# Kernel optimization log

Measured on AMD Instinct MI355X. Metric: run time of the kernel, lower is better.

The kernel has to match this reference:

```python
import jax, jax.numpy as jnp
import numpy as np

B, S, F = 4, 2048, 8
D, H, L, FF = 256, 8, 2, 1024
DH = D // H
NSK, NPAT = 2000, 64
DQ = D // 4  # pattern/feat sub-embedding width


def setup_inputs() -> dict:
    key = jax.random.key(0)
    ks = jax.random.split(key, 32)
    r = lambda i, shape: jax.random.normal(ks[i], shape, jnp.float32) * 0.02
    return {
        'interactions': jax.random.randint(ks[0], (B, S), 0, 2 * NSK),
        'patterns': jax.random.randint(ks[1], (B, S), 0, NPAT),
        'forget_features': jax.random.normal(ks[2], (B, S, F), jnp.float32),
        'inter_emb': r(3, (2 * NSK, D)),
        'pattern_emb': r(4, (NPAT, DQ)),
        'feat_W': r(5, (F, DQ)), 'feat_b': jnp.zeros((DQ,), jnp.float32),
        'in_W': r(6, (D + 2 * DQ, D)), 'in_b': jnp.zeros((D,), jnp.float32),
        'time_W': r(7, (1, D)), 'time_b': jnp.zeros((D,), jnp.float32),
        'pos_W': r(8, (1, D)), 'pos_b': jnp.zeros((D,), jnp.float32),
        'Wq': r(9, (L, D, H, DH)), 'bq': jnp.zeros((L, H, DH), jnp.float32),
        'Wk': r(10, (L, D, H, DH)), 'bk': jnp.zeros((L, H, DH), jnp.float32),
        'Wv': r(11, (L, D, H, DH)), 'bv': jnp.zeros((L, H, DH), jnp.float32),
        'Wo': r(12, (L, H, DH, D)), 'bo': jnp.zeros((L, D), jnp.float32),
        'kerple_p': jnp.full((L, H, 1, 1), 0.5, jnp.float32),
        'kerple_a': jnp.zeros((L, H, 1, 1), jnp.float32),
        'ln1_g': jnp.ones((L, D), jnp.float32), 'ln1_b': jnp.zeros((L, D), jnp.float32),
        'ln2_g': jnp.ones((L, D), jnp.float32), 'ln2_b': jnp.zeros((L, D), jnp.float32),
        'ffn_W1': r(13, (L, D, FF)), 'ffn_b1': jnp.zeros((L, FF), jnp.float32),
        'ffn_W2': r(14, (L, FF, D)), 'ffn_b2': jnp.zeros((L, D), jnp.float32),
        'out_W': r(15, (D, NSK)), 'out_b': jnp.zeros((NSK,), jnp.float32),
    }


def _ln(x, g, b, eps=1e-6):
    m = jnp.mean(x, -1, keepdims=True)
    v = jnp.mean(jnp.square(x - m), -1, keepdims=True)
    return g * (x - m) * jax.lax.rsqrt(v + eps) + b


def reference(interactions, patterns, forget_features, inter_emb, pattern_emb,
              feat_W, feat_b, in_W, in_b, time_W, time_b, pos_W, pos_b,
              Wq, bq, Wk, bk, Wv, bv, Wo, bo, kerple_p, kerple_a,
              ln1_g, ln1_b, ln2_g, ln2_b, ffn_W1, ffn_b1, ffn_W2, ffn_b2,
              out_W, out_b):
    inter_e = inter_emb[interactions]                      # [B,S,D]
    pat_e = pattern_emb[patterns]                          # [B,S,D/4]
    feat_e = forget_features @ feat_W + feat_b             # [B,S,D/4]
    x = jnp.concatenate([inter_e, pat_e, feat_e], -1) @ in_W + in_b  # [B,S,D]
    elapsed = forget_features[:, :, 0:1]
    time_enc = jnp.tanh(elapsed @ time_W + time_b)
    pos = jnp.arange(S, dtype=jnp.float32)[None, :, None] / jnp.float32(S)
    pos_enc = pos @ pos_W + pos_b
    x = x + time_enc + pos_enc

    positions = jnp.arange(S, dtype=jnp.float32)
    dist = jnp.maximum(positions[:, None] - positions[None, :], 0.0)  # [S,S]
    causal_bias = jnp.triu(jnp.full((S, S), -1e9, jnp.float32), 1)    # [S,S]
    inv_sqrt_dh = 1.0 / jnp.sqrt(jnp.float32(DH))

    for i in range(L):
        p = jax.nn.softplus(kerple_p[i])                   # [H,1,1]
        a = jax.nn.softplus(kerple_a[i])
        bias = causal_bias[None] - p * jnp.log1p(a * dist[None])  # [H,S,S]
        q = jnp.einsum('bsd,dhk->bshk', x, Wq[i]) + bq[i]
        k = jnp.einsum('bsd,dhk->bshk', x, Wk[i]) + bk[i]
        v = jnp.einsum('bsd,dhk->bshk', x, Wv[i]) + bv[i]
        scores = jnp.einsum('bshk,bthk->bhst', q, k) * inv_sqrt_dh + bias[None]
        attn = jax.nn.softmax(scores, axis=-1)
        o = jnp.einsum('bhst,bthk->bshk', attn, v)
        attn_out = jnp.einsum('bshk,hkd->bsd', o, Wo[i]) + bo[i]
        x = _ln(x + attn_out, ln1_g[i], ln1_b[i])
        h = jax.nn.gelu(x @ ffn_W1[i] + ffn_b1[i], approximate=False)
        ffn_out = h @ ffn_W2[i] + ffn_b2[i]
        x = _ln(x + ffn_out, ln2_g[i], ln2_b[i])
    return x @ out_W + out_b
```

## Files before the change

kernel.cpp:

```cpp
#include <hip/hip_runtime.h>
#include <math.h>

#define SEQ   2048
#define BATCH 4
#define NTOK  8192
#define DM    256
#define NHD   8
#define DHD   32
#define DFF   1024
#define NSKC  2000

typedef __attribute__((ext_vector_type(8))) short short8;
typedef __attribute__((ext_vector_type(4))) float f32x4;
typedef unsigned short ushort_t;

__device__ __forceinline__ ushort_t f2bf(float x) {
    union { float f; unsigned u; } c; c.f = x;
    unsigned r = c.u + 0x7FFFu + ((c.u >> 16) & 1u);
    return (ushort_t)(r >> 16);
}

struct ConvSeg { const float* src; ushort_t* dst; int K; int N; int Npad; };
struct ConvArgs { ConvSeg s[14]; };

__global__ __launch_bounds__(256) void convert_kernel(ConvArgs args) {
    ConvSeg sg = args.s[blockIdx.y];
    int e = blockIdx.x * 256 + threadIdx.x;
    int tot = sg.Npad * sg.K;
    if (e >= tot) return;
    int n = e / sg.K;
    int k = e - n * sg.K;
    float v = (n < sg.N) ? sg.src[(size_t)k * sg.N + n] : 0.0f;
    sg.dst[e] = f2bf(v);
}

__global__ __launch_bounds__(384) void concat_kernel(
    const int* __restrict__ interactions, const int* __restrict__ patterns,
    const float* __restrict__ ff, const float* __restrict__ inter_emb,
    const float* __restrict__ pattern_emb, const float* __restrict__ feat_W,
    const float* __restrict__ feat_b, ushort_t* __restrict__ out)
{
    int tok = blockIdx.x;
    int j = threadIdx.x;
    float v;
    if (j < 256) {
        v = inter_emb[(size_t)interactions[tok] * 256 + j];
    } else if (j < 320) {
        v = pattern_emb[patterns[tok] * 64 + (j - 256)];
    } else {
        int c = j - 320;
        float acc = feat_b[c];
#pragma unroll
        for (int f = 0; f < 8; f++) acc += ff[tok * 8 + f] * feat_W[f * 64 + c];
        v = acc;
    }
    out[(size_t)tok * 384 + j] = f2bf(v);
}

__global__ __launch_bounds__(256) void addenc_kernel(
    float* __restrict__ x, ushort_t* __restrict__ xb, const float* __restrict__ ff,
    const float* __restrict__ time_W, const float* __restrict__ time_b,
    const float* __restrict__ pos_W, const float* __restrict__ pos_b)
{
    int tok = blockIdx.x;
    int d = threadIdx.x;
    int s = tok & (SEQ - 1);
    float el = ff[tok * 8];
    float te = tanhf(el * time_W[d] + time_b[d]);
    float pe = ((float)s * (1.0f / (float)SEQ)) * pos_W[d] + pos_b[d];
    size_t idx = (size_t)tok * DM + d;
    float nv = x[idx] + te + pe;
    x[idx] = nv;
    xb[idx] = f2bf(nv);
}

__global__ __launch_bounds__(256) void ln_kernel(
    float* __restrict__ x, const float* __restrict__ r,
    const float* __restrict__ g, const float* __restrict__ b,
    ushort_t* __restrict__ xb)
{
    int tok = blockIdx.x;
    int d = threadIdx.x;
    size_t idx = (size_t)tok * DM + d;
    float v = x[idx] + r[idx];
    float s1 = v, s2 = v * v;
#pragma unroll
    for (int off = 32; off > 0; off >>= 1) {
        s1 += __shfl_down(s1, off, 64);
        s2 += __shfl_down(s2, off, 64);
    }
    __shared__ float red1[4], red2[4];
    int wid = d >> 6, lane = d & 63;
    if (lane == 0) { red1[wid] = s1; red2[wid] = s2; }
    __syncthreads();
    s1 = red1[0] + red1[1] + red1[2] + red1[3];
    s2 = red2[0] + red2[1] + red2[2] + red2[3];
    float mean = s1 * (1.0f / 256.0f);
    float var = s2 * (1.0f / 256.0f) - mean * mean;
    float inv = rsqrtf(var + 1e-6f);
    float nv = g[d] * (v - mean) * inv + b[d];
    x[idx] = nv;
    xb[idx] = f2bf(nv);
}

__global__ __launch_bounds__(256) void gemm_bf16(
    const ushort_t* __restrict__ A, const ushort_t* __restrict__ Bt,
    int M, int N, int K, int mode,
    float* __restrict__ Cf, ushort_t* __restrict__ Cb,
    ushort_t* __restrict__ Ck, ushort_t* __restrict__ Cv,
    const float* __restrict__ b0, const float* __restrict__ b1,
    const float* __restrict__ b2)
{
    __shared__ ushort_t As[128][40];
    __shared__ ushort_t Bs[64][40];
    int m0 = blockIdx.y * 128, n0 = blockIdx.x * 64;
    int tid = threadIdx.x;
    int wv = tid >> 6, lane = tid & 63;
    int quad = lane >> 4, l16 = lane & 15;
    int srow = tid >> 2, sc = (tid & 3) << 3;

    f32x4 acc[2][4];
#pragma unroll
    for (int i = 0; i < 2; i++)
#pragma unroll
        for (int j = 0; j < 4; j++) acc[i][j] = (f32x4){0.f, 0.f, 0.f, 0.f};

    uint4 pa0 = *(const uint4*)&A[(size_t)(m0 + srow) * K + sc];
    uint4 pa1 = *(const uint4*)&A[(size_t)(m0 + 64 + srow) * K + sc];
    uint4 pbb = *(const uint4*)&Bt[(size_t)(n0 + srow) * K + sc];

    int msub = wv * 32;
    for (int k0 = 0; k0 < K; k0 += 32) {
        __syncthreads();
        *(uint4*)&As[srow][sc] = pa0;
        *(uint4*)&As[64 + srow][sc] = pa1;
        *(uint4*)&Bs[srow][sc] = pbb;
        __syncthreads();
        if (k0 + 32 < K) {
            pa0 = *(const uint4*)&A[(size_t)(m0 + srow) * K + k0 + 32 + sc];
            pa1 = *(const uint4*)&A[(size_t)(m0 + 64 + srow) * K + k0 + 32 + sc];
            pbb = *(const uint4*)&Bt[(size_t)(n0 + srow) * K + k0 + 32 + sc];
        }
        short8 af0 = *(const short8*)&As[msub + l16][quad * 8];
        short8 af1 = *(const short8*)&As[msub + 16 + l16][quad * 8];
        short8 bf0 = *(const short8*)&Bs[l16][quad * 8];
        short8 bf1 = *(const short8*)&Bs[16 + l16][quad * 8];
        short8 bf2 = *(const short8*)&Bs[32 + l16][quad * 8];
        short8 bf3 = *(const short8*)&Bs[48 + l16][quad * 8];
        acc[0][0] = __builtin_amdgcn_mfma_f32_16x16x32_bf16(af0, bf0, acc[0][0], 0, 0, 0);
        acc[0][1] = __builtin_amdgcn_mfma_f32_16x16x32_bf16(af0, bf1, acc[0][1], 0, 0, 0);
        acc[0][2] = __builtin_amdgcn_mfma_f32_16x16x32_bf16(af0, bf2, acc[0][2], 0, 0, 0);
        acc[0][3] = __builtin_amdgcn_mfma_f32_16x16x32_bf16(af0, bf3, acc[0][3], 0, 0, 0);
        acc[1][0] = __builtin_amdgcn_mfma_f32_16x16x32_bf16(af1, bf0, acc[1][0], 0, 0, 0);
        acc[1][1] = __builtin_amdgcn_mfma_f32_16x16x32_bf16(af1, bf1, acc[1][1], 0, 0, 0);
        acc[1][2] = __builtin_amdgcn_mfma_f32_16x16x32_bf16(af1, bf2, acc[1][2], 0, 0, 0);
        acc[1][3] = __builtin_amdgcn_mfma_f32_16x16x32_bf16(af1, bf3, acc[1][3], 0, 0, 0);
    }

#pragma unroll
    for (int mt = 0; mt < 2; mt++) {
#pragma unroll
        for (int nt = 0; nt < 4; nt++) {
            int n = n0 + nt * 16 + l16;
#pragma unroll
            for (int r = 0; r < 4; r++) {
                int m = m0 + msub + mt * 16 + quad * 4 + r;
                float v = acc[mt][nt][r];
                if (mode == 0) {
                    Cf[(size_t)m * N + n] = v + b0[n];
                } else {
                    int which = n >> 8, idx = n & 255;
                    int hh = idx >> 5, d = idx & 31;
                    int s = m & (SEQ - 1), b = m >> 11;
                    if (which == 0)
                        Cb[(((size_t)(b * NHD + hh)) * SEQ + s) * DHD + d] = f2bf(v + b0[idx]);
                    else if (which == 1)
                        Ck[(((size_t)(b * NHD + hh)) * SEQ + s) * DHD + d] = f2bf(v + b1[idx]);
                    else
                        Cv[(((size_t)(b * NHD + hh)) * DHD + d) * SEQ + s] = f2bf(v + b2[idx]);
                }
            }
        }
    }
}

__global__ __launch_bounds__(256) void gemm_bf16_128(
    const ushort_t* __restrict__ A, const ushort_t* __restrict__ Bt,
    int M, int N, int K, int mode,
    float* __restrict__ Cf, ushort_t* __restrict__ Cb,
    const float* __restrict__ b0, int Nreal)
{
    __shared__ ushort_t As[128][40];
    __shared__ ushort_t Bs[128][40];
    int m0 = blockIdx.y * 128, n0 = blockIdx.x * 128;
    int tid = threadIdx.x;
    int wv = tid >> 6, lane = tid & 63;
    int quad = lane >> 4, l16 = lane & 15;
    int wm = (wv >> 1) * 64, wn = (wv & 1) * 64;
    int srow = tid >> 1, sc = (tid & 1) << 4;

    f32x4 acc[4][4];
#pragma unroll
    for (int i = 0; i < 4; i++)
#pragma unroll
        for (int j = 0; j < 4; j++) acc[i][j] = (f32x4){0.f, 0.f, 0.f, 0.f};

    uint4 pa0 = *(const uint4*)&A[(size_t)(m0 + srow) * K + sc];
    uint4 pa1 = *(const uint4*)&A[(size_t)(m0 + srow) * K + sc + 8];
    uint4 pb0 = *(const uint4*)&Bt[(size_t)(n0 + srow) * K + sc];
    uint4 pb1 = *(const uint4*)&Bt[(size_t)(n0 + srow) * K + sc + 8];

    for (int k0 = 0; k0 < K; k0 += 32) {
        __syncthreads();
        *(uint4*)&As[srow][sc] = pa0;
        *(uint4*)&As[srow][sc + 8] = pa1;
        *(uint4*)&Bs[srow][sc] = pb0;
        *(uint4*)&Bs[srow][sc + 8] = pb1;
        __syncthreads();
        if (k0 + 32 < K) {
            pa0 = *(const uint4*)&A[(size_t)(m0 + srow) * K + k0 + 32 + sc];
            pa1 = *(const uint4*)&A[(size_t)(m0 + srow) * K + k0 + 32 + sc + 8];
            pb0 = *(const uint4*)&Bt[(size_t)(n0 + srow) * K + k0 + 32 + sc];
            pb1 = *(const uint4*)&Bt[(size_t)(n0 + srow) * K + k0 + 32 + sc + 8];
        }
        short8 af[4], bf[4];
#pragma unroll
        for (int i = 0; i < 4; i++) {
            af[i] = *(const short8*)&As[wm + i * 16 + l16][quad * 8];
            bf[i] = *(const short8*)&Bs[wn + i * 16 + l16][quad * 8];
        }
#pragma unroll
        for (int i = 0; i < 4; i++)
#pragma unroll
            for (int j = 0; j < 4; j++)
                acc[i][j] = __builtin_amdgcn_mfma_f32_16x16x32_bf16(af[i], bf[j], acc[i][j], 0, 0, 0);
    }

#pragma unroll
    for (int i = 0; i < 4; i++) {
#pragma unroll
        for (int j = 0; j < 4; j++) {
            int n = n0 + wn + j * 16 + l16;
#pragma unroll
            for (int r = 0; r < 4; r++) {
                int m = m0 + wm + i * 16 + quad * 4 + r;
                float v = acc[i][j][r];
                if (mode == 1) {
                    float t = v + b0[n];
                    t = 0.5f * t * (1.0f + erff(t * 0.70710678118654752f));
                    Cb[(size_t)m * N + n] = f2bf(t);
                } else {
                    if (n < Nreal) Cf[(size_t)m * Nreal + n] = v + b0[n];
                }
            }
        }
    }
}

__global__ __launch_bounds__(256) void attn_mfma(
    const ushort_t* __restrict__ qb, const ushort_t* __restrict__ kb,
    const ushort_t* __restrict__ vtb, const float* __restrict__ kp,
    const float* __restrict__ ka, ushort_t* __restrict__ ob)
{
    int h = blockIdx.y, b = blockIdx.z;
    int tid = threadIdx.x, wv = tid >> 6, lane = tid & 63;
    int quad = lane >> 4, l16 = lane & 15;
    __shared__ float tab[SEQ];
    __shared__ ushort_t P[4][2][16 * 40];

    float pp = log1pf(__expf(kp[h]));
    float aa = log1pf(__expf(ka[h]));
    for (int i = tid; i < SEQ; i += 256) tab[i] = -pp * log1pf(aa * (float)i);
    __syncthreads();

    int bh = b * NHD + h;
    const ushort_t* Qh = qb + (size_t)bh * SEQ * DHD;
    const ushort_t* Kh = kb + (size_t)bh * SEQ * DHD;
    const ushort_t* Vh = vtb + (size_t)bh * DHD * SEQ;

    int j = blockIdx.x * 4 + wv;
    int tlo = j, thi = 127 - j;
    int qlo0 = tlo * 16, qhi0 = thi * 16;
    const float scale = 0.17677669529663687f;

    short8 qfl = *(const short8*)&Qh[(qlo0 + l16) * DHD + quad * 8];
    short8 qfh = *(const short8*)&Qh[(qhi0 + l16) * DHD + quad * 8];
    f32x4 ol0 = (f32x4){0.f,0.f,0.f,0.f}, ol1 = (f32x4){0.f,0.f,0.f,0.f};
    f32x4 oh0 = (f32x4){0.f,0.f,0.f,0.f}, oh1 = (f32x4){0.f,0.f,0.f,0.f};
    float lsl[4] = {0.f,0.f,0.f,0.f}, lsh[4] = {0.f,0.f,0.f,0.f};
    ushort_t* Pl = &P[wv][0][0];
    ushort_t* Ph = &P[wv][1][0];

    int nch_hi = (thi + 2) >> 1;
    int nch_lo = (tlo + 2) >> 1;
    int qsrh = qhi0 + quad * 4;
    int qsrl = qlo0 + quad * 4;

    for (int ch = 0; ch < nch_hi; ch++) {
        int k0 = ch * 32;
        short8 kf0 = *(const short8*)&Kh[(k0 + l16) * DHD + quad * 8];
        short8 kf1 = *(const short8*)&Kh[(k0 + 16 + l16) * DHD + quad * 8];
        short8 vf0 = *(const short8*)&Vh[l16 * SEQ + k0 + quad * 8];
        short8 vf1 = *(const short8*)&Vh[(16 + l16) * SEQ + k0 + quad * 8];
        f32x4 z = (f32x4){0.f,0.f,0.f,0.f};

        f32x4 s0 = __builtin_amdgcn_mfma_f32_16x16x32_bf16(qfh, kf0, z, 0, 0, 0);
        f32x4 s1 = __builtin_amdgcn_mfma_f32_16x16x32_bf16(qfh, kf1, z, 0, 0, 0);
        if (k0 + 31 <= qhi0) {
#pragma unroll
            for (int r = 0; r < 4; r++) {
                const float* tp = &tab[qsrh + r - k0 - l16 - 16];
                float e0 = __expf(s0[r] * scale + tp[16]);
                float e1 = __expf(s1[r] * scale + tp[0]);
                lsh[r] += e0 + e1;
                Ph[(quad * 4 + r) * 40 + l16]      = f2bf(e0);
                Ph[(quad * 4 + r) * 40 + 16 + l16] = f2bf(e1);
            }
        } else {
#pragma unroll
            for (int r = 0; r < 4; r++) {
                int d0 = qsrh + r - k0 - l16;
                int d1 = d0 - 16;
                float e0 = 0.f, e1 = 0.f;
                if (d0 >= 0) e0 = __expf(s0[r] * scale + tab[d0]);
                if (d1 >= 0) e1 = __expf(s1[r] * scale + tab[d1]);
                lsh[r] += e0 + e1;
                Ph[(quad * 4 + r) * 40 + l16]      = f2bf(e0);
                Ph[(quad * 4 + r) * 40 + 16 + l16] = f2bf(e1);
            }
        }

        bool do_lo = (ch < nch_lo);
        if (do_lo) {
            f32x4 t0 = __builtin_amdgcn_mfma_f32_16x16x32_bf16(qfl, kf0, z, 0, 0, 0);
            f32x4 t1 = __builtin_amdgcn_mfma_f32_16x16x32_bf16(qfl, kf1, z, 0, 0, 0);
            if (k0 + 31 <= qlo0) {
#pragma unroll
                for (int r = 0; r < 4; r++) {
                    const float* tp = &tab[qsrl + r - k0 - l16 - 16];
                    float e0 = __expf(t0[r] * scale + tp[16]);
                    float e1 = __expf(t1[r] * scale + tp[0]);
                    lsl[r] += e0 + e1;
                    Pl[(quad * 4 + r) * 40 + l16]      = f2bf(e0);
                    Pl[(quad * 4 + r) * 40 + 16 + l16] = f2bf(e1);
                }
            } else {
#pragma unroll
                for (int r = 0; r < 4; r++) {
                    int d0 = qsrl + r - k0 - l16;
                    int d1 = d0 - 16;
                    float e0 = 0.f, e1 = 0.f;
                    if (d0 >= 0) e0 = __expf(t0[r] * scale + tab[d0]);
                    if (d1 >= 0) e1 = __expf(t1[r] * scale + tab[d1]);
                    lsl[r] += e0 + e1;
                    Pl[(quad * 4 + r) * 40 + l16]      = f2bf(e0);
                    Pl[(quad * 4 + r) * 40 + 16 + l16] = f2bf(e1);
                }
            }
        }

        __builtin_amdgcn_s_waitcnt(0xC07F);
        __builtin_amdgcn_wave_barrier();
        short8 pfh = *(const short8*)&Ph[l16 * 40 + quad * 8];
        oh0 = __builtin_amdgcn_mfma_f32_16x16x32_bf16(pfh, vf0, oh0, 0, 0, 0);
        oh1 = __builtin_amdgcn_mfma_f32_16x16x32_bf16(pfh, vf1, oh1, 0, 0, 0);
        if (do_lo) {
            short8 pfl = *(const short8*)&Pl[l16 * 40 + quad * 8];
            ol0 = __builtin_amdgcn_mfma_f32_16x16x32_bf16(pfl, vf0, ol0, 0, 0, 0);
            ol1 = __builtin_amdgcn_mfma_f32_16x16x32_bf16(pfl, vf1, ol1, 0, 0, 0);
        }
    }

#pragma unroll
    for (int r = 0; r < 4; r++) {
#pragma unroll
        for (int off = 1; off < 16; off <<= 1) {
            lsh[r] += __shfl_xor(lsh[r], off, 16);
            lsl[r] += __shfl_xor(lsl[r], off, 16);
        }
    }
#pragma unroll
    for (int r = 0; r < 4; r++) {
        float rh = 1.0f / lsh[r];
        float rl = 1.0f / lsl[r];
        size_t bh_ = ((size_t)(b * SEQ + qsrh + r)) * DM + h * DHD;
        size_t bl_ = ((size_t)(b * SEQ + qsrl + r)) * DM + h * DHD;
        ob[bh_ + l16]      = f2bf(oh0[r] * rh);
        ob[bh_ + 16 + l16] = f2bf(oh1[r] * rh);
        ob[bl_ + l16]      = f2bf(ol0[r] * rl);
        ob[bl_ + 16 + l16] = f2bf(ol1[r] * rl);
    }
}

extern "C" void kernel_launch(void* const* d_in, const int* in_sizes, int n_in,
                              void* d_out, int out_size, void* d_ws, size_t ws_size,
                              hipStream_t stream) {
    const int*   interactions = (const int*)d_in[0];
    const int*   patterns     = (const int*)d_in[1];
    const float* ff           = (const float*)d_in[2];
    const float* inter_emb    = (const float*)d_in[3];
    const float* pattern_emb  = (const float*)d_in[4];
    const float* feat_W       = (const float*)d_in[5];
    const float* feat_b       = (const float*)d_in[6];
    const float* in_W         = (const float*)d_in[7];
    const float* in_b         = (const float*)d_in[8];
    const float* time_W       = (const float*)d_in[9];
    const float* time_b       = (const float*)d_in[10];
    const float* pos_W        = (const float*)d_in[11];
    const float* pos_b        = (const float*)d_in[12];
    const float* Wq           = (const float*)d_in[13];
    const float* bq           = (const float*)d_in[14];
    const float* Wk           = (const float*)d_in[15];
    const float* bk           = (const float*)d_in[16];
    const float* Wv           = (const float*)d_in[17];
    const float* bv           = (const float*)d_in[18];
    const float* Wo           = (const float*)d_in[19];
    const float* bo           = (const float*)d_in[20];
    const float* kerple_p     = (const float*)d_in[21];
    const float* kerple_a     = (const float*)d_in[22];
    const float* ln1_g        = (const float*)d_in[23];
    const float* ln1_b        = (const float*)d_in[24];
    const float* ln2_g        = (const float*)d_in[25];
    const float* ln2_b        = (const float*)d_in[26];
    const float* ffn_W1       = (const float*)d_in[27];
    const float* ffn_b1       = (const float*)d_in[28];
    const float* ffn_W2       = (const float*)d_in[29];
    const float* ffn_b2       = (const float*)d_in[30];
    const float* out_W        = (const float*)d_in[31];
    const float* out_b        = (const float*)d_in[32];
    float* out = (float*)d_out;

    char* wsb = (char*)d_ws;
    const size_t MB = 1024 * 1024;
    float*    x    = (float*)(wsb + 0);
    float*    tmp  = (float*)(wsb + 8  * MB);
    ushort_t* xb   = (ushort_t*)(wsb + 16 * MB);
    ushort_t* qbuf = (ushort_t*)(wsb + 20 * MB);
    ushort_t* kbuf = (ushort_t*)(wsb + 24 * MB);
    ushort_t* vtbf = (ushort_t*)(wsb + 28 * MB);
    ushort_t* shrd = (ushort_t*)(wsb + 32 * MB);
    ushort_t* cbuf = shrd;
    ushort_t* o_bf = shrd;
    ushort_t* h_bf = shrd;
    char* wp = wsb + 48 * MB;
    ushort_t* inWt  = (ushort_t*)wp;  wp += 256  * 384 * 2;
    ushort_t* qkvWt = (ushort_t*)wp;  wp += 2 * 768 * 256 * 2;
    ushort_t* WoT   = (ushort_t*)wp;  wp += 2 * 256 * 256 * 2;
    ushort_t* W1T   = (ushort_t*)wp;  wp += 2 * 1024 * 256 * 2;
    ushort_t* W2T   = (ushort_t*)wp;  wp += 2 * 256 * 1024 * 2;
    ushort_t* outWt = (ushort_t*)wp;  wp += 2048 * 256 * 2;

    ConvArgs ca;
    int D2 = 256 * 256;
    ca.s[0]  = { in_W,              inWt,               384,  256,  256 };
    ca.s[1]  = { Wq,                qkvWt,              256,  256,  256 };
    ca.s[2]  = { Wk,                qkvWt + 1 * D2,     256,  256,  256 };
    ca.s[3]  = { Wv,                qkvWt + 2 * D2,     256,  256,  256 };
    ca.s[4]  = { Wq + D2,           qkvWt + 3 * D2,     256,  256,  256 };
    ca.s[5]  = { Wk + D2,           qkvWt + 4 * D2,     256,  256,  256 };
    ca.s[6]  = { Wv + D2,           qkvWt + 5 * D2,     256,  256,  256 };
    ca.s[7]  = { Wo,                WoT,                256,  256,  256 };
    ca.s[8]  = { Wo + D2,           WoT + D2,           256,  256,  256 };
    ca.s[9]  = { ffn_W1,            W1T,                256,  1024, 1024 };
    ca.s[10] = { ffn_W1 + 4 * D2,   W1T + 4 * D2,       256,  1024, 1024 };
    ca.s[11] = { ffn_W2,            W2T,                1024, 256,  256 };
    ca.s[12] = { ffn_W2 + 4 * D2,   W2T + 4 * D2,       1024, 256,  256 };
    ca.s[13] = { out_W,             outWt,              256,  2000, 2048 };
    convert_kernel<<<dim3(2048, 14), 256, 0, stream>>>(ca);

    concat_kernel<<<NTOK, 384, 0, stream>>>(interactions, patterns, ff,
                                            inter_emb, pattern_emb, feat_W, feat_b, cbuf);
    gemm_bf16<<<dim3(4, 64), 256, 0, stream>>>(cbuf, inWt, NTOK, 256, 384, 0,
                                               x, nullptr, nullptr, nullptr,
                                               in_b, nullptr, nullptr);
    addenc_kernel<<<NTOK, 256, 0, stream>>>(x, xb, ff, time_W, time_b, pos_W, pos_b);

    for (int l = 0; l < 2; l++) {
        gemm_bf16<<<dim3(12, 64), 256, 0, stream>>>(
            xb, qkvWt + (size_t)l * 768 * 256, NTOK, 768, 256, 2,
            nullptr, qbuf, kbuf, vtbf,
            bq + l * 256, bk + l * 256, bv + l * 256);
        attn_mfma<<<dim3(16, NHD, BATCH), 256, 0, stream>>>(
            qbuf, kbuf, vtbf, kerple_p + l * NHD, kerple_a + l * NHD, o_bf);
        gemm_bf16<<<dim3(4, 64), 256, 0, stream>>>(
            o_bf, WoT + (size_t)l * D2, NTOK, 256, 256, 0,
            tmp, nullptr, nullptr, nullptr, bo + l * 256, nullptr, nullptr);
        ln_kernel<<<NTOK, 256, 0, stream>>>(x, tmp, ln1_g + l * 256, ln1_b + l * 256, xb);
        gemm_bf16_128<<<dim3(8, 64), 256, 0, stream>>>(
            xb, W1T + (size_t)l * 4 * D2, NTOK, 1024, 256, 1,
            nullptr, h_bf, ffn_b1 + l * 1024, 1024);
        gemm_bf16<<<dim3(4, 64), 256, 0, stream>>>(
            h_bf, W2T + (size_t)l * 4 * D2, NTOK, 256, 1024, 0,
            tmp, nullptr, nullptr, nullptr, ffn_b2 + l * 256, nullptr, nullptr);
        ln_kernel<<<NTOK, 256, 0, stream>>>(x, tmp, ln2_g + l * 256, ln2_b + l * 256, xb);
    }

    gemm_bf16_128<<<dim3(16, 64), 256, 0, stream>>>(
        xb, outWt, NTOK, 2048, 256, 3,
        out, nullptr, out_b, NSKC);
}
```

Measured before the change: 488.6 us.

## Tile weight transpose, move QKV to 128-wide GEMM, compute kerple bias inline with exp2

The weight conversion kernel now transposes 32x32 tiles through shared memory, so both the fp32 reads and the bf16 writes are coalesced. The QKV projection moves to the 128x128 GEMM, which folds the softmax scale and log2(e) into Q and writes V with a permuted sequence order. Attention drops the shared-memory bias table and computes the kerple bias per element with log2/exp2. It also merges the interior and edge paths using a predicated mask and packs two bf16 P values per store. The trade is extra transcendental math per score in exchange for fewer table loads, fewer LDS stores and fewer GEMM blocks.

Measured after the change: 488.7 us. Within noise of the previous version (+0.0%).

```diff
diff --git a/kernel.cpp b/kernel.cpp
--- a/kernel.cpp
+++ b/kernel.cpp
@@ -14,6 +14,8 @@
 typedef __attribute__((ext_vector_type(4))) float f32x4;
 typedef unsigned short ushort_t;
 
+#define QPRE ((float)(0.17677669529663687 * 1.4426950408889634))
+
 __device__ __forceinline__ ushort_t f2bf(float x) {
     union { float f; unsigned u; } c; c.f = x;
     unsigned r = c.u + 0x7FFFu + ((c.u >> 16) & 1u);
@@ -24,14 +26,26 @@
 struct ConvArgs { ConvSeg s[14]; };
 
 __global__ __launch_bounds__(256) void convert_kernel(ConvArgs args) {
-    ConvSeg sg = args.s[blockIdx.y];
-    int e = blockIdx.x * 256 + threadIdx.x;
-    int tot = sg.Npad * sg.K;
-    if (e >= tot) return;
-    int n = e / sg.K;
-    int k = e - n * sg.K;
-    float v = (n < sg.N) ? sg.src[(size_t)k * sg.N + n] : 0.0f;
-    sg.dst[e] = f2bf(v);
+    ConvSeg sg = args.s[blockIdx.z];
+    int n0 = blockIdx.x * 32, k0 = blockIdx.y * 32;
+    if (n0 >= sg.Npad || k0 >= sg.K) return;
+    __shared__ float T[32][33];
+    int tid = threadIdx.x;
+    int tn = tid & 31, tk4 = tid >> 5;
+#pragma unroll
+    for (int i = 0; i < 4; i++) {
+        int kl = tk4 + i * 8;
+        float v = 0.0f;
+        if (n0 + tn < sg.N) v = sg.src[(size_t)(k0 + kl) * sg.N + n0 + tn];
+        T[kl][tn] = v;
+    }
+    __syncthreads();
+    int tk = tid & 31, tn4 = tid >> 5;
+#pragma unroll
+    for (int i = 0; i < 4; i++) {
+        int nl = tn4 + i * 8;
+        sg.dst[(size_t)(n0 + nl) * sg.K + k0 + tk] = f2bf(T[tk][nl]);
+    }
 }
 
 __global__ __launch_bounds__(384) void concat_kernel(
@@ -105,11 +119,8 @@
 
 __global__ __launch_bounds__(256) void gemm_bf16(
     const ushort_t* __restrict__ A, const ushort_t* __restrict__ Bt,
-    int M, int N, int K, int mode,
-    float* __restrict__ Cf, ushort_t* __restrict__ Cb,
-    ushort_t* __restrict__ Ck, ushort_t* __restrict__ Cv,
-    const float* __restrict__ b0, const float* __restrict__ b1,
-    const float* __restrict__ b2)
+    int M, int N, int K,
+    float* __restrict__ Cf, const float* __restrict__ b0)
 {
     __shared__ ushort_t As[128][40];
     __shared__ ushort_t Bs[64][40];
@@ -165,20 +176,7 @@
 #pragma unroll
             for (int r = 0; r < 4; r++) {
                 int m = m0 + msub + mt * 16 + quad * 4 + r;
-                float v = acc[mt][nt][r];
-                if (mode == 0) {
-                    Cf[(size_t)m * N + n] = v + b0[n];
-                } else {
-                    int which = n >> 8, idx = n & 255;
-                    int hh = idx >> 5, d = idx & 31;
-                    int s = m & (SEQ - 1), b = m >> 11;
-                    if (which == 0)
-                        Cb[(((size_t)(b * NHD + hh)) * SEQ + s) * DHD + d] = f2bf(v + b0[idx]);
-                    else if (which == 1)
-                        Ck[(((size_t)(b * NHD + hh)) * SEQ + s) * DHD + d] = f2bf(v + b1[idx]);
-                    else
-                        Cv[(((size_t)(b * NHD + hh)) * DHD + d) * SEQ + s] = f2bf(v + b2[idx]);
-                }
+                Cf[(size_t)m * N + n] = acc[mt][nt][r] + b0[n];
             }
         }
     }
@@ -188,7 +186,9 @@
     const ushort_t* __restrict__ A, const ushort_t* __restrict__ Bt,
     int M, int N, int K, int mode,
     float* __restrict__ Cf, ushort_t* __restrict__ Cb,
-    const float* __restrict__ b0, int Nreal)
+    ushort_t* __restrict__ Ck, ushort_t* __restrict__ Cv,
+    const float* __restrict__ b0, const float* __restrict__ b1,
+    const float* __restrict__ b2, int Nreal)
 {
     __shared__ ushort_t As[128][40];
     __shared__ ushort_t Bs[128][40];
@@ -249,8 +249,21 @@
                     float t = v + b0[n];
                     t = 0.5f * t * (1.0f + erff(t * 0.70710678118654752f));
                     Cb[(size_t)m * N + n] = f2bf(t);
+                } else if (mode == 3) {
+                    if (n < Nreal) Cf[(size_t)m * Nreal + n] = v + b0[n];
                 } else {
-                    if (n < Nreal) Cf[(size_t)m * Nreal + n] = v + b0[n];
+                    int which = n >> 8, idx = n & 255;
+                    int hh = idx >> 5, d = idx & 31;
+                    int s = m & (SEQ - 1), b = m >> 11;
+                    if (which == 0)
+                        Cb[(((size_t)(b * NHD + hh)) * SEQ + s) * DHD + d] =
+                            f2bf((v + b0[idx]) * QPRE);
+                    else if (which == 1)
+                        Ck[(((size_t)(b * NHD + hh)) * SEQ + s) * DHD + d] = f2bf(v + b1[idx]);
+                    else {
+                        int sp = (s & ~31) | (((s & 15) << 1) | ((s >> 4) & 1));
+                        Cv[(((size_t)(b * NHD + hh)) * DHD + d) * SEQ + sp] = f2bf(v + b2[idx]);
+                    }
                 }
             }
         }
@@ -265,13 +278,10 @@
     int h = blockIdx.y, b = blockIdx.z;
     int tid = threadIdx.x, wv = tid >> 6, lane = tid & 63;
     int quad = lane >> 4, l16 = lane & 15;
-    __shared__ float tab[SEQ];
-    __shared__ ushort_t P[4][2][16 * 40];
-
-    float pp = log1pf(__expf(kp[h]));
-    float aa = log1pf(__expf(ka[h]));
-    for (int i = tid; i < SEQ; i += 256) tab[i] = -pp * log1pf(aa * (float)i);
-    __syncthreads();
+    __shared__ ushort_t P2[4][2][16 * 40];
+
+    float p = log1pf(__expf(kp[h]));
+    float a = log1pf(__expf(ka[h]));
 
     int bh = b * NHD + h;
     const ushort_t* Qh = qb + (size_t)bh * SEQ * DHD;
@@ -281,15 +291,14 @@
     int j = blockIdx.x * 4 + wv;
     int tlo = j, thi = 127 - j;
     int qlo0 = tlo * 16, qhi0 = thi * 16;
-    const float scale = 0.17677669529663687f;
 
     short8 qfl = *(const short8*)&Qh[(qlo0 + l16) * DHD + quad * 8];
     short8 qfh = *(const short8*)&Qh[(qhi0 + l16) * DHD + quad * 8];
     f32x4 ol0 = (f32x4){0.f,0.f,0.f,0.f}, ol1 = (f32x4){0.f,0.f,0.f,0.f};
     f32x4 oh0 = (f32x4){0.f,0.f,0.f,0.f}, oh1 = (f32x4){0.f,0.f,0.f,0.f};
     float lsl[4] = {0.f,0.f,0.f,0.f}, lsh[4] = {0.f,0.f,0.f,0.f};
-    ushort_t* Pl = &P[wv][0][0];
-    ushort_t* Ph = &P[wv][1][0];
+    ushort_t* Pl = &P2[wv][0][0];
+    ushort_t* Ph = &P2[wv][1][0];
 
     int nch_hi = (thi + 2) >> 1;
     int nch_lo = (tlo + 2) >> 1;
@@ -306,27 +315,21 @@
 
         f32x4 s0 = __builtin_amdgcn_mfma_f32_16x16x32_bf16(qfh, kf0, z, 0, 0, 0);
         f32x4 s1 = __builtin_amdgcn_mfma_f32_16x16x32_bf16(qfh, kf1, z, 0, 0, 0);
-        if (k0 + 31 <= qhi0) {
+        {
+            float df = (float)(qsrh - k0 - l16);
+            bool interior = (k0 + 31 <= qhi0);
 #pragma unroll
             for (int r = 0; r < 4; r++) {
-                const float* tp = &tab[qsrh + r - k0 - l16 - 16];
-                float e0 = __expf(s0[r] * scale + tp[16]);
-                float e1 = __expf(s1[r] * scale + tp[0]);
+                float d0 = df + (float)r, d1 = d0 - 16.0f;
+                float e0 = exp2f(s0[r] - p * __log2f(fmaf(a, d0, 1.0f)));
+                float e1 = exp2f(s1[r] - p * __log2f(fmaf(a, d1, 1.0f)));
+                if (!interior) {
+                    e0 = (d0 >= 0.0f) ? e0 : 0.0f;
+                    e1 = (d1 >= 0.0f) ? e1 : 0.0f;
+                }
                 lsh[r] += e0 + e1;
-                Ph[(quad * 4 + r) * 40 + l16]      = f2bf(e0);
-                Ph[(quad * 4 + r) * 40 + 16 + l16] = f2bf(e1);
-            }
-        } else {
-#pragma unroll
-            for (int r = 0; r < 4; r++) {
-                int d0 = qsrh + r - k0 - l16;
-                int d1 = d0 - 16;
-                float e0 = 0.f, e1 = 0.f;
-                if (d0 >= 0) e0 = __expf(s0[r] * scale + tab[d0]);
-                if (d1 >= 0) e1 = __expf(s1[r] * scale + tab[d1]);
-                lsh[r] += e0 + e1;
-                Ph[(quad * 4 + r) * 40 + l16]      = f2bf(e0);
-                Ph[(quad * 4 + r) * 40 + 16 + l16] = f2bf(e1);
+                unsigned pk = (unsigned)f2bf(e0) | ((unsigned)f2bf(e1) << 16);
+                *(unsigned*)&Ph[(quad * 4 + r) * 40 + l16 * 2] = pk;
             }
         }
 
@@ -334,28 +337,20 @@
         if (do_lo) {
             f32x4 t0 = __builtin_amdgcn_mfma_f32_16x16x32_bf16(qfl, kf0, z, 0, 0, 0);
             f32x4 t1 = __builtin_amdgcn_mfma_f32_16x16x32_bf16(qfl, kf1, z, 0, 0, 0);
-            if (k0 + 31 <= qlo0) {
-#pragma unroll
-                for (int r = 0; r < 4; r++) {
-                    const float* tp = &tab[qsrl + r - k0 - l16 - 16];
-                    float e0 = __expf(t0[r] * scale + tp[16]);
-                    float e1 = __expf(t1[r] * scale + tp[0]);
-                    lsl[r] += e0 + e1;
-                    Pl[(quad * 4 + r) * 40 + l16]      = f2bf(e0);
-                    Pl[(quad * 4 + r) * 40 + 16 + l16] = f2bf(e1);
+            float df = (float)(qsrl - k0 - l16);
+            bool interior = (k0 + 31 <= qlo0);
+#pragma unroll
+            for (int r = 0; r < 4; r++) {
+                float d0 = df + (float)r, d1 = d0 - 16.0f;
+                float e0 = exp2f(t0[r] - p * __log2f(fmaf(a, d0, 1.0f)));
+                float e1 = exp2f(t1[r] - p * __log2f(fmaf(a, d1, 1.0f)));
+                if (!interior) {
+                    e0 = (d0 >= 0.0f) ? e0 : 0.0f;
+                    e1 = (d1 >= 0.0f) ? e1 : 0.0f;
                 }
-            } else {
-#pragma unroll
-                for (int r = 0; r < 4; r++) {
-                    int d0 = qsrl + r - k0 - l16;
-                    int d1 = d0 - 16;
-                    float e0 = 0.f, e1 = 0.f;
-                    if (d0 >= 0) e0 = __expf(t0[r] * scale + tab[d0]);
-                    if (d1 >= 0) e1 = __expf(t1[r] * scale + tab[d1]);
-                    lsl[r] += e0 + e1;
-                    Pl[(quad * 4 + r) * 40 + l16]      = f2bf(e0);
-                    Pl[(quad * 4 + r) * 40 + 16 + l16] = f2bf(e1);
-                }
+                lsl[r] += e0 + e1;
+                unsigned pk = (unsigned)f2bf(e0) | ((unsigned)f2bf(e1) << 16);
+                *(unsigned*)&Pl[(quad * 4 + r) * 40 + l16 * 2] = pk;
             }
         }
 
@@ -466,36 +461,32 @@
     ca.s[11] = { ffn_W2,            W2T,                1024, 256,  256 };
     ca.s[12] = { ffn_W2 + 4 * D2,   W2T + 4 * D2,       1024, 256,  256 };
     ca.s[13] = { out_W,             outWt,              256,  2000, 2048 };
-    convert_kernel<<<dim3(2048, 14), 256, 0, stream>>>(ca);
+    convert_kernel<<<dim3(64, 32, 14), 256, 0, stream>>>(ca);
 
     concat_kernel<<<NTOK, 384, 0, stream>>>(interactions, patterns, ff,
                                             inter_emb, pattern_emb, feat_W, feat_b, cbuf);
-    gemm_bf16<<<dim3(4, 64), 256, 0, stream>>>(cbuf, inWt, NTOK, 256, 384, 0,
-                                               x, nullptr, nullptr, nullptr,
-                                               in_b, nullptr, nullptr);
+    gemm_bf16<<<dim3(4, 64), 256, 0, stream>>>(cbuf, inWt, NTOK, 256, 384, x, in_b);
     addenc_kernel<<<NTOK, 256, 0, stream>>>(x, xb, ff, time_W, time_b, pos_W, pos_b);
 
     for (int l = 0; l < 2; l++) {
-        gemm_bf16<<<dim3(12, 64), 256, 0, stream>>>(
+        gemm_bf16_128<<<dim3(6, 64), 256, 0, stream>>>(
             xb, qkvWt + (size_t)l * 768 * 256, NTOK, 768, 256, 2,
             nullptr, qbuf, kbuf, vtbf,
-            bq + l * 256, bk + l * 256, bv + l * 256);
+            bq + l * 256, bk + l * 256, bv + l * 256, 0);
         attn_mfma<<<dim3(16, NHD, BATCH), 256, 0, stream>>>(
             qbuf, kbuf, vtbf, kerple_p + l * NHD, kerple_a + l * NHD, o_bf);
         gemm_bf16<<<dim3(4, 64), 256, 0, stream>>>(
-            o_bf, WoT + (size_t)l * D2, NTOK, 256, 256, 0,
-            tmp, nullptr, nullptr, nullptr, bo + l * 256, nullptr, nullptr);
+            o_bf, WoT + (size_t)l * D2, NTOK, 256, 256, tmp, bo + l * 256);
         ln_kernel<<<NTOK, 256, 0, stream>>>(x, tmp, ln1_g + l * 256, ln1_b + l * 256, xb);
         gemm_bf16_128<<<dim3(8, 64), 256, 0, stream>>>(
             xb, W1T + (size_t)l * 4 * D2, NTOK, 1024, 256, 1,
-            nullptr, h_bf, ffn_b1 + l * 1024, 1024);
+            nullptr, h_bf, nullptr, nullptr, ffn_b1 + l * 1024, nullptr, nullptr, 0);
         gemm_bf16<<<dim3(4, 64), 256, 0, stream>>>(
-            h_bf, W2T + (size_t)l * 4 * D2, NTOK, 256, 1024, 0,
-            tmp, nullptr, nullptr, nullptr, ffn_b2 + l * 256, nullptr, nullptr);
+            h_bf, W2T + (size_t)l * 4 * D2, NTOK, 256, 1024, tmp, ffn_b2 + l * 256);
         ln_kernel<<<NTOK, 256, 0, stream>>>(x, tmp, ln2_g + l * 256, ln2_b + l * 256, xb);
     }
 
     gemm_bf16_128<<<dim3(16, 64), 256, 0, stream>>>(
         xb, outWt, NTOK, 2048, 256, 3,
-        out, nullptr, out_b, NSKC);
-}
+        out, nullptr, nullptr, nullptr, out_b, nullptr, nullptr, NSKC);
+}
```
